# Optimization experiments

Hardware: AMD Instinct MI355X
Metric: run time of the kernel (lower is better)

Reference implementation:

```python
import jax, jax.numpy as jnp
import numpy as np

B, T, C, H = 2, 2048, 1024, 16
HD = C // H  # head dim = 64


def setup_inputs() -> dict:
    key = jax.random.key(0)
    k0, k1, k2 = jax.random.split(key, 3)
    x = jax.random.normal(k0, (B, T, C), jnp.float32)
    W_attn = jax.random.normal(k1, (C, 3 * C), jnp.float32) * 0.02
    b_attn = jnp.zeros((3 * C,), jnp.float32)
    W_proj = jax.random.normal(k2, (C, C), jnp.float32) * 0.02
    b_proj = jnp.zeros((C,), jnp.float32)
    # causal mask, broadcast over (B, H) like torch masked_fill(~mask)
    attn_mask = jnp.tril(jnp.ones((T, T), dtype=bool))[None, None]
    return {"x": x, "W_attn": W_attn, "b_attn": b_attn,
            "W_proj": W_proj, "b_proj": b_proj, "attn_mask": attn_mask}


def _rotate_half(x):
    # interleaved rotate_half as in rotary-embedding-torch: (x1,x2)->(-x2,x1)
    x1 = x[..., 0::2]
    x2 = x[..., 1::2]
    return jnp.stack((-x2, x1), axis=-1).reshape(x.shape)


def _apply_rope(x):
    # x: [B, H, T, HD]
    hd = x.shape[-1]
    t = x.shape[-2]
    inv_freq = 1.0 / (10000.0 ** (jnp.arange(0, hd, 2, dtype=jnp.float32) / hd))
    freqs = jnp.arange(t, dtype=jnp.float32)[:, None] * inv_freq[None, :]  # [T, HD/2]
    freqs = jnp.repeat(freqs, 2, axis=-1)  # [T, HD], interleaved
    return x * jnp.cos(freqs) + _rotate_half(x) * jnp.sin(freqs)


def reference(x, W_attn, b_attn, W_proj, b_proj, attn_mask):
    Bb, Tt, Cc = x.shape
    qkv = x @ W_attn + b_attn                     # [B, T, 3C]
    q, k, v = jnp.split(qkv, 3, axis=-1)

    def to_heads(z):
        return z.reshape(Bb, Tt, H, HD).transpose(0, 2, 1, 3)  # [B, H, T, HD]

    q, k, v = to_heads(q), to_heads(k), to_heads(v)
    q = _apply_rope(q)
    k = _apply_rope(k)

    scale = 1.0 / jnp.sqrt(jnp.float32(HD))
    att = jnp.einsum('bhqd,bhkd->bhqk', q, k) * scale  # [B, H, T, T]
    att = jnp.where(attn_mask, att, jnp.float32(-10000.0))
    att = jax.nn.softmax(att, axis=-1)
    # dropout = 0.0 (eval): identity
    y = jnp.einsum('bhqk,bhkd->bhqd', att, v)           # [B, H, T, HD]
    y = y.transpose(0, 2, 1, 3).reshape(Bb, Tt, Cc)
    return y @ W_proj + b_proj
```

## Files before the change

kernel.cpp:

```cpp
#include <hip/hip_runtime.h>

#define B_ 2
#define T_ 2048
#define C_ 1024
#define H_ 16
#define HD_ 64

typedef unsigned short u16;
typedef unsigned int u32;
typedef __attribute__((ext_vector_type(8))) short short8;
typedef __attribute__((ext_vector_type(4))) float f32x4;
typedef __attribute__((ext_vector_type(2))) u32 uint2v;
typedef __attribute__((ext_vector_type(4))) u32 uint4v;

typedef __attribute__((address_space(1))) const void* as1cv;
typedef __attribute__((address_space(3))) void* as3v;

__device__ __forceinline__ u16 f2bf(float x){
  union { float f; u32 u; } v; v.f = x;
  u32 r = v.u + 0x7fffu + ((v.u >> 16) & 1u);
  return (u16)(r >> 16);
}
__device__ __forceinline__ float bf2f(u16 h){
  union { u32 u; float f; } v; v.u = ((u32)h) << 16;
  return v.f;
}
__device__ __forceinline__ u32 cvt_pk_bf16(float lo, float hi){
  u32 r;
  asm("v_cvt_pk_bf16_f32 %0, %1, %2" : "=v"(r) : "v"(lo), "v"(hi));
  return r;
}
__device__ __forceinline__ void gl_lds16(const u16* src, u16* dst){
  __builtin_amdgcn_global_load_lds((as1cv)src, (as3v)dst, 16, 0, 0);
}

__global__ void k_conv(const float* __restrict__ in, u16* __restrict__ out){
  int i = blockIdx.x * 256 + threadIdx.x;
  f32x4 v = ((const f32x4*)in)[i];
  uint2v o;
  o.x = (u32)f2bf(v.x) | ((u32)f2bf(v.y) << 16);
  o.y = (u32)f2bf(v.z) | ((u32)f2bf(v.w) << 16);
  ((uint2v*)out)[i] = o;
}

__global__ void k_transpose(const float* __restrict__ in, u16* __restrict__ out,
                            int R, int Cc){
  __shared__ float tile[32][33];
  int c0 = blockIdx.x * 32, r0 = blockIdx.y * 32;
  int tx = threadIdx.x, ty = threadIdx.y;
#pragma unroll
  for (int ii = 0; ii < 4; ++ii)
    tile[ty + ii*8][tx] = in[(size_t)(r0 + ty + ii*8) * Cc + c0 + tx];
  __syncthreads();
#pragma unroll
  for (int ii = 0; ii < 4; ++ii)
    out[(size_t)(c0 + ty + ii*8) * R + r0 + tx] = f2bf(tile[tx][ty + ii*8]);
}

__global__ __launch_bounds__(256, 2)
void k_gemm0(const u16* __restrict__ A, const u16* __restrict__ Bt,
             const float* __restrict__ bias, u16* __restrict__ Qh,
             u16* __restrict__ Kh, u16* __restrict__ vt,
             int M, int N, int K)
{
  __shared__ u16 As[128*64];
  __shared__ u16 Bs[128*64];
  int nwg = gridDim.x;
  int cpx = nwg >> 3;
  int bid = blockIdx.x;
  int wg = (bid & 7) * cpx + (bid >> 3);
  int ntn = N >> 7;
  int m0 = (wg / ntn) << 7, n0 = (wg % ntn) << 7;
  int tid = threadIdx.x;
  int lane = tid & 63, w = tid >> 6;
  int c = lane & 15, g = lane >> 4;
  int wr = w >> 1, wc = w & 1;

  f32x4 z4 = {0.f,0.f,0.f,0.f};
  f32x4 acc[4][4];
#pragma unroll
  for (int i=0;i<4;++i)
#pragma unroll
    for (int j=0;j<4;++j) acc[i][j] = z4;

  u16* dstA = As + ((tid & 0xC0) << 3);
  u16* dstB = Bs + ((tid & 0xC0) << 3);

  for (int k0 = 0; k0 < K; k0 += 64){
#pragma unroll
    for (int it = 0; it < 4; ++it){
      int ch = it*256 + tid;
      int row = ch >> 3, slot = ch & 7;
      gl_lds16(A + (size_t)(m0+row)*K + k0 + slot*8, dstA + it*2048);
    }
#pragma unroll
    for (int it = 0; it < 4; ++it){
      int ch = it*256 + tid;
      int row = ch >> 3, slot = ch & 7;
      gl_lds16(Bt + (size_t)(n0+row)*K + k0 + slot*8, dstB + it*2048);
    }
    __syncthreads();
#pragma unroll
    for (int ks = 0; ks < 2; ++ks){
      short8 af[4], bf[4];
#pragma unroll
      for (int i=0;i<4;++i)
        af[i] = *(const short8*)(As + (wr*64 + i*16 + c)*64 + ks*32 + g*8);
#pragma unroll
      for (int j=0;j<4;++j)
        bf[j] = *(const short8*)(Bs + (wc*64 + j*16 + c)*64 + ks*32 + g*8);
#pragma unroll
      for (int i=0;i<4;++i)
#pragma unroll
        for (int j=0;j<4;++j)
          acc[i][j] = __builtin_amdgcn_mfma_f32_16x16x32_bf16(af[i], bf[j], acc[i][j], 0, 0, 0);
    }
    __syncthreads();
  }

  if (n0 >= 2048){
#pragma unroll
    for (int i=0;i<4;++i){
      int rowb = m0 + wr*64 + i*16 + g*4;
      int bb = rowb >> 11, t0 = rowb & 2047;
#pragma unroll
      for (int j=0;j<4;++j){
        int col = n0 + wc*64 + j*16 + c;
        float bv = bias[col];
        int vc = col - 2048;
        int hh = vc >> 6, d = vc & 63;
        uint2v o;
        o.x = (u32)f2bf(acc[i][j].x + bv) | ((u32)f2bf(acc[i][j].y + bv) << 16);
        o.y = (u32)f2bf(acc[i][j].z + bv) | ((u32)f2bf(acc[i][j].w + bv) << 16);
        *(uint2v*)(vt + ((size_t)((bb*16 + hh)*64 + d))*2048 + t0) = o;
      }
    }
  } else {
    bool isQ = (n0 < 1024);
    u16* dsth = isQ ? Qh : Kh;
    int colb = isQ ? n0 : (n0 - 1024);
    float qsc = isQ ? 0.180336880f : 1.0f;
    float sgn = (c & 1) ? 1.f : -1.f;
#pragma unroll
    for (int nf=0; nf<4; ++nf){
      int scol = colb + wc*64 + nf*16 + c;
      int hh = scol >> 6, d = scol & 63;
      int ip = (d >> 1);
      float invr = exp2f((float)(-ip) * 0.4152410118609203f) * 0.15915494309f;
      float bv = bias[n0 + wc*64 + nf*16 + c];
      u16* base = dsth + (size_t)hh*2048*64 + d;
#pragma unroll
      for (int mf=0; mf<4; ++mf){
#pragma unroll
        for (int r=0; r<4; ++r){
          int row = m0 + wr*64 + mf*16 + g*4 + r;
          int t = row & 2047, b = row >> 11;
          float v = acc[mf][nf][r] + bv;
          float p = __shfl_xor(v, 1);
          float th = (float)t * invr;
          float fr = th - floorf(th);
          float sn = __builtin_amdgcn_sinf(fr);
          float cs = __builtin_amdgcn_cosf(fr);
          float y = (v*cs + p*sn*sgn) * qsc;
          base[((size_t)b*16*2048 + t)*64] = f2bf(y);
        }
      }
    }
  }
}

__global__ __launch_bounds__(256, 2)
void k_gemmp(const u16* __restrict__ A, const u16* __restrict__ Bt,
             const float* __restrict__ bias, float* __restrict__ outf)
{
  __shared__ u16 As[128*64];
  __shared__ u16 Bs[64*64];
  const int K = 1024, N = 1024;
  int nwg = gridDim.x;
  int cpx = nwg >> 3;
  int bid = blockIdx.x;
  int wg = (bid & 7) * cpx + (bid >> 3);
  int m0 = (wg >> 4) << 7, n0 = (wg & 15) << 6;
  int tid = threadIdx.x;
  int lane = tid & 63, w = tid >> 6;
  int c = lane & 15, g = lane >> 4;
  int wr = w >> 1, wc = w & 1;

  f32x4 z4 = {0.f,0.f,0.f,0.f};
  f32x4 acc[4][2];
#pragma unroll
  for (int i=0;i<4;++i)
#pragma unroll
    for (int j=0;j<2;++j) acc[i][j] = z4;

  u16* dstA = As + ((tid & 0xC0) << 3);
  u16* dstB = Bs + ((tid & 0xC0) << 3);

  for (int k0 = 0; k0 < K; k0 += 64){
#pragma unroll
    for (int it = 0; it < 4; ++it){
      int ch = it*256 + tid;
      int row = ch >> 3, slot = ch & 7;
      gl_lds16(A + (size_t)(m0+row)*K + k0 + slot*8, dstA + it*2048);
    }
#pragma unroll
    for (int it = 0; it < 2; ++it){
      int ch = it*256 + tid;
      int row = ch >> 3, slot = ch & 7;
      gl_lds16(Bt + (size_t)(n0+row)*K + k0 + slot*8, dstB + it*2048);
    }
    __syncthreads();
#pragma unroll
    for (int ks = 0; ks < 2; ++ks){
      short8 af[4], bf[2];
#pragma unroll
      for (int i=0;i<4;++i)
        af[i] = *(const short8*)(As + (wr*64 + i*16 + c)*64 + ks*32 + g*8);
#pragma unroll
      for (int j=0;j<2;++j)
        bf[j] = *(const short8*)(Bs + (wc*32 + j*16 + c)*64 + ks*32 + g*8);
#pragma unroll
      for (int i=0;i<4;++i)
#pragma unroll
        for (int j=0;j<2;++j)
          acc[i][j] = __builtin_amdgcn_mfma_f32_16x16x32_bf16(af[i], bf[j], acc[i][j], 0, 0, 0);
    }
    __syncthreads();
  }

#pragma unroll
  for (int i=0;i<4;++i){
#pragma unroll
    for (int j=0;j<2;++j){
      int col = n0 + wc*32 + j*16 + c;
      float bv = bias[col];
#pragma unroll
      for (int r=0;r<4;++r){
        int row = m0 + wr*64 + i*16 + g*4 + r;
        outf[(size_t)row*N + col] = acc[i][j][r] + bv;
      }
    }
  }
}

__global__ __launch_bounds__(256, 3)
void k_attn(const u16* __restrict__ Qh, const u16* __restrict__ Kh,
            const u16* __restrict__ Vt, u16* __restrict__ Pb,
            float* __restrict__ lp)
{
  __shared__ u16 KV[4*4096];
  __shared__ u16 Ps[4*32*64];

  int bid = blockIdx.x;
  int qt = 15 - (bid >> 7);
  int r7 = bid & 127;
  int ck = r7 >> 5, bh = r7 & 31;
  int q0 = qt << 7;
  int tid = threadIdx.x, lane = tid & 63, w = tid >> 6;
  int c = lane & 15, g = lane >> 4;
  int q0w = q0 + w*32;
  int nt = (qt + 1) << 1;
  int t0 = (nt * ck) >> 2;
  int t1 = (nt * (ck + 1)) >> 2;

  const u16* Kbase = Kh + (size_t)bh * T_ * 64;
  const u16* Vbase = Vt + (size_t)bh * 64 * T_;
  const u16* Qbase = Qh + (size_t)bh * T_ * 64;

  short8 qf[2][2];
#pragma unroll
  for (int qs=0;qs<2;++qs)
#pragma unroll
    for (int ks=0;ks<2;++ks)
      qf[qs][ks] = *(const short8*)(Qbase + (size_t)(q0w + qs*16 + c)*64 + ks*32 + g*8);

  f32x4 z4 = {0.f,0.f,0.f,0.f};
  f32x4 acc[2][4];
#pragma unroll
  for (int qs=0;qs<2;++qs)
#pragma unroll
    for (int ds=0;ds<4;++ds) acc[qs][ds] = z4;
  float psum[2] = {0.f, 0.f};

  char* PsB = (char*)Ps + w*4096;

  int row2[2], soff2[2];
  u16* dst0[2];
#pragma unroll
  for (int it=0; it<2; ++it){
    int ch = it*256 + tid;
    row2[it] = ch >> 3;
    int slot = ch & 7;
    soff2[it] = (slot ^ (row2[it] & 7)) << 3;
    dst0[it] = KV + ((it*256 + (tid & 0xC0)) << 3);
  }

  if (t0 < t1){
    int kv0 = t0 << 6;
#pragma unroll
    for (int it=0; it<2; ++it){
      gl_lds16(Kbase + (size_t)(kv0 + row2[it])*64 + soff2[it], dst0[it]);
      gl_lds16(Vbase + (size_t)row2[it]*T_ + kv0 + soff2[it], dst0[it] + 2*4096);
    }
  }
  __syncthreads();

  for (int t = t0; t < t1; ++t){
    int cur = (t - t0) & 1;
    int kv0 = t << 6;
    if (t + 1 < t1){
      int kvn = kv0 + 64;
      int nxt = cur ^ 1;
#pragma unroll
      for (int it=0; it<2; ++it){
        gl_lds16(Kbase + (size_t)(kvn + row2[it])*64 + soff2[it], dst0[it] + nxt*4096);
        gl_lds16(Vbase + (size_t)row2[it]*T_ + kvn + soff2[it], dst0[it] + (2+nxt)*4096);
      }
    }

    if (kv0 <= q0w + 31){
      const char* KsC = (const char*)(KV + cur*4096);
      const char* VsC = (const char*)(KV + (2+cur)*4096);

      f32x4 st[4][2];
#pragma unroll
      for (int kv=0;kv<4;++kv)
#pragma unroll
        for (int qs=0;qs<2;++qs) st[kv][qs] = z4;

#pragma unroll
      for (int ks=0;ks<2;++ks){
        short8 kf[4];
#pragma unroll
        for (int kv=0;kv<4;++kv){
          int row = kv*16 + c;
          kf[kv] = *(const short8*)(KsC + row*128 + (((ks*4+g) ^ (row&7)) << 4));
        }
#pragma unroll
        for (int kv=0;kv<4;++kv)
#pragma unroll
          for (int qs=0;qs<2;++qs)
            st[kv][qs] = __builtin_amdgcn_mfma_f32_16x16x32_bf16(kf[kv], qf[qs][ks], st[kv][qs], 0, 0, 0);
      }

      if (kv0 + 63 > q0w){
#pragma unroll
        for (int kv=0;kv<4;++kv)
#pragma unroll
          for (int qs=0;qs<2;++qs)
#pragma unroll
            for (int r=0;r<4;++r){
              int kvi = kv0 + kv*16 + g*4 + r;
              int qi = q0w + qs*16 + c;
              if (kvi > qi) st[kv][qs][r] = -INFINITY;
            }
      }

#pragma unroll
      for (int qs=0;qs<2;++qs){
        float s01 = 0.f, s23 = 0.f;
#pragma unroll
        for (int kv=0;kv<4;++kv){
          float e0 = __builtin_amdgcn_exp2f(st[kv][qs][0]);
          float e1 = __builtin_amdgcn_exp2f(st[kv][qs][1]);
          float e2 = __builtin_amdgcn_exp2f(st[kv][qs][2]);
          float e3 = __builtin_amdgcn_exp2f(st[kv][qs][3]);
          st[kv][qs][0] = e0; st[kv][qs][1] = e1;
          st[kv][qs][2] = e2; st[kv][qs][3] = e3;
          s01 += e0 + e1; s23 += e2 + e3;
        }
        psum[qs] += s01 + s23;
        int q = qs*16 + c;
#pragma unroll
        for (int kv=0;kv<4;++kv){
          uint2v o;
          o.x = cvt_pk_bf16(st[kv][qs][0], st[kv][qs][1]);
          o.y = cvt_pk_bf16(st[kv][qs][2], st[kv][qs][3]);
          *(uint2v*)(PsB + q*128 + ((kv*32 + g*8) ^ ((q&7) << 4))) = o;
        }
      }

#pragma unroll
      for (int ks=0;ks<2;++ks){
        short8 vb[4];
#pragma unroll
        for (int ds=0;ds<4;++ds){
          int row = ds*16 + c;
          vb[ds] = *(const short8*)(VsC + row*128 + (((ks*4+g) ^ (row&7)) << 4));
        }
#pragma unroll
        for (int qs=0;qs<2;++qs){
          int q = qs*16 + c;
          short8 pa = *(const short8*)(PsB + q*128 + (((ks*4+g) << 4) ^ ((q&7) << 4)));
#pragma unroll
          for (int ds=0;ds<4;++ds)
            acc[qs][ds] = __builtin_amdgcn_mfma_f32_16x16x32_bf16(pa, vb[ds], acc[qs][ds], 0, 0, 0);
        }
      }
    }

    __syncthreads();
  }

#pragma unroll
  for (int qs=0;qs<2;++qs){
    psum[qs] += __shfl_xor(psum[qs], 16);
    psum[qs] += __shfl_xor(psum[qs], 32);
  }
  if (g == 0){
    lp[ck*65536 + bh*2048 + q0w + c]      = psum[0];
    lp[ck*65536 + bh*2048 + q0w + 16 + c] = psum[1];
  }
#pragma unroll
  for (int qs=0;qs<2;++qs){
#pragma unroll
    for (int r=0;r<4;++r){
      int trow = q0w + qs*16 + g*4 + r;
      size_t off = (((size_t)(ck*32 + bh)*2048) + trow)*64;
#pragma unroll
      for (int ds=0;ds<4;++ds)
        Pb[off + ds*16 + c] = f2bf(acc[qs][ds][r]);
    }
  }
}

__global__ void k_merge(const u16* __restrict__ Pb, const float* __restrict__ lp,
                        u16* __restrict__ Y)
{
  int idx = blockIdx.x * 256 + threadIdx.x;
  int d8 = idx & 7;
  int t  = (idx >> 3) & 2047;
  int bh = idx >> 14;
  int lt = bh*2048 + t;
  float l = lp[lt] + lp[lt + 65536] + lp[lt + 131072] + lp[lt + 196608];
  float inv = 1.0f / l;
  float s[8] = {0.f,0.f,0.f,0.f,0.f,0.f,0.f,0.f};
#pragma unroll
  for (int ck=0; ck<4; ++ck){
    short8 p = *(const short8*)(Pb + (((size_t)(ck*32 + bh)*2048 + t) << 6) + d8*8);
#pragma unroll
    for (int j=0;j<8;++j) s[j] += bf2f((u16)p[j]);
  }
  uint4v o;
  o.x = cvt_pk_bf16(s[0]*inv, s[1]*inv);
  o.y = cvt_pk_bf16(s[2]*inv, s[3]*inv);
  o.z = cvt_pk_bf16(s[4]*inv, s[5]*inv);
  o.w = cvt_pk_bf16(s[6]*inv, s[7]*inv);
  int bb = bh >> 4, hh = bh & 15;
  *(uint4v*)(Y + ((size_t)(bb*2048 + t))*1024 + hh*64 + d8*8) = o;
}

extern "C" void kernel_launch(void* const* d_in, const int* in_sizes, int n_in,
                              void* d_out, int out_size, void* d_ws, size_t ws_size,
                              hipStream_t stream)
{
  const float* x  = (const float*)d_in[0];
  const float* Wa = (const float*)d_in[1];
  const float* ba = (const float*)d_in[2];
  const float* Wp = (const float*)d_in[3];
  const float* bp = (const float*)d_in[4];
  float* out = (float*)d_out;
  char* ws = (char*)d_ws;

  u16* xb  = (u16*)(ws);
  u16* WaT = (u16*)(ws + (8u  << 20));
  u16* Pb  = (u16*)(ws);
  u16* Qh  = (u16*)(ws + (32u << 20));
  u16* Y   = Qh;
  u16* Kh  = (u16*)(ws + (40u << 20));
  u16* Vt  = (u16*)(ws + (48u << 20));
  u16* WpT = (u16*)(ws + (56u << 20));
  float* lp = (float*)(ws + (58u << 20));

  k_conv<<<4096, 256, 0, stream>>>(x, xb);
  k_transpose<<<dim3(96,32), dim3(32,8), 0, stream>>>(Wa, WaT, 1024, 3072);
  k_transpose<<<dim3(32,32), dim3(32,8), 0, stream>>>(Wp, WpT, 1024, 1024);
  k_gemm0<<<768, 256, 0, stream>>>(xb, WaT, ba, Qh, Kh, Vt, 4096, 3072, 1024);
  k_attn<<<2048, 256, 0, stream>>>(Qh, Kh, Vt, Pb, lp);
  k_merge<<<2048, 256, 0, stream>>>(Pb, lp, Y);
  k_gemmp<<<512, 256, 0, stream>>>(Y, WpT, bp, out);
}
```

Baseline: 111.3 us.

## Double-buffer LDS in both GEMMs and widen projection GEMM tile to 128x128

Both the QKV GEMM and the output-projection GEMM now use two LDS buffers. The next K-slice is loaded from global memory into one buffer while MFMAs consume the other, which removes one barrier per iteration and hides load latency. The projection GEMM also moves from 128x64 to 128x128 tiles with half as many workgroups, which raises operand reuse. In exchange, LDS use doubles to 64KB per block, which may lower occupancy, and the projection launch has only 256 workgroups to spread across the CUs.

```diff
diff --git a/kernel.cpp b/kernel.cpp
--- a/kernel.cpp
+++ b/kernel.cpp
@@ -63,8 +63,7 @@
              u16* __restrict__ Kh, u16* __restrict__ vt,
              int M, int N, int K)
 {
-  __shared__ u16 As[128*64];
-  __shared__ u16 Bs[128*64];
+  __shared__ u16 LDSG[32768];
   int nwg = gridDim.x;
   int cpx = nwg >> 3;
   int bid = blockIdx.x;
@@ -83,23 +82,38 @@
 #pragma unroll
     for (int j=0;j<4;++j) acc[i][j] = z4;
 
-  u16* dstA = As + ((tid & 0xC0) << 3);
-  u16* dstB = Bs + ((tid & 0xC0) << 3);
-
-  for (int k0 = 0; k0 < K; k0 += 64){
-#pragma unroll
-    for (int it = 0; it < 4; ++it){
-      int ch = it*256 + tid;
-      int row = ch >> 3, slot = ch & 7;
-      gl_lds16(A + (size_t)(m0+row)*K + k0 + slot*8, dstA + it*2048);
-    }
-#pragma unroll
-    for (int it = 0; it < 4; ++it){
-      int ch = it*256 + tid;
-      int row = ch >> 3, slot = ch & 7;
-      gl_lds16(Bt + (size_t)(n0+row)*K + k0 + slot*8, dstB + it*2048);
-    }
-    __syncthreads();
+  int rowS[4], slotS[4], dstS[4];
+#pragma unroll
+  for (int it=0; it<4; ++it){
+    int ch = it*256 + tid;
+    rowS[it] = ch >> 3;
+    slotS[it] = (ch & 7) * 8;
+    dstS[it] = it*2048 + ((tid & 0xC0) << 3);
+  }
+  const u16* Abase = A + (size_t)m0*K;
+  const u16* Bbase = Bt + (size_t)n0*K;
+
+#pragma unroll
+  for (int it=0; it<4; ++it){
+    gl_lds16(Abase + (size_t)rowS[it]*K + slotS[it], LDSG + dstS[it]);
+    gl_lds16(Bbase + (size_t)rowS[it]*K + slotS[it], LDSG + 16384 + dstS[it]);
+  }
+  __syncthreads();
+
+  int nk = K >> 6;
+  for (int kt = 0; kt < nk; ++kt){
+    int cur = kt & 1;
+    if (kt + 1 < nk){
+      int k1 = (kt + 1) << 6;
+      int nb = cur ^ 1;
+#pragma unroll
+      for (int it=0; it<4; ++it){
+        gl_lds16(Abase + (size_t)rowS[it]*K + k1 + slotS[it], LDSG + nb*8192 + dstS[it]);
+        gl_lds16(Bbase + (size_t)rowS[it]*K + k1 + slotS[it], LDSG + 16384 + nb*8192 + dstS[it]);
+      }
+    }
+    const u16* As = LDSG + cur*8192;
+    const u16* Bs = LDSG + 16384 + cur*8192;
 #pragma unroll
     for (int ks = 0; ks < 2; ++ks){
       short8 af[4], bf[4];
@@ -173,56 +187,70 @@
 void k_gemmp(const u16* __restrict__ A, const u16* __restrict__ Bt,
              const float* __restrict__ bias, float* __restrict__ outf)
 {
-  __shared__ u16 As[128*64];
-  __shared__ u16 Bs[64*64];
+  __shared__ u16 LDSG[32768];
   const int K = 1024, N = 1024;
   int nwg = gridDim.x;
   int cpx = nwg >> 3;
   int bid = blockIdx.x;
   int wg = (bid & 7) * cpx + (bid >> 3);
-  int m0 = (wg >> 4) << 7, n0 = (wg & 15) << 6;
+  int m0 = (wg >> 3) << 7, n0 = (wg & 7) << 7;
   int tid = threadIdx.x;
   int lane = tid & 63, w = tid >> 6;
   int c = lane & 15, g = lane >> 4;
   int wr = w >> 1, wc = w & 1;
 
   f32x4 z4 = {0.f,0.f,0.f,0.f};
-  f32x4 acc[4][2];
+  f32x4 acc[4][4];
 #pragma unroll
   for (int i=0;i<4;++i)
 #pragma unroll
-    for (int j=0;j<2;++j) acc[i][j] = z4;
-
-  u16* dstA = As + ((tid & 0xC0) << 3);
-  u16* dstB = Bs + ((tid & 0xC0) << 3);
-
-  for (int k0 = 0; k0 < K; k0 += 64){
-#pragma unroll
-    for (int it = 0; it < 4; ++it){
-      int ch = it*256 + tid;
-      int row = ch >> 3, slot = ch & 7;
-      gl_lds16(A + (size_t)(m0+row)*K + k0 + slot*8, dstA + it*2048);
-    }
-#pragma unroll
-    for (int it = 0; it < 2; ++it){
-      int ch = it*256 + tid;
-      int row = ch >> 3, slot = ch & 7;
-      gl_lds16(Bt + (size_t)(n0+row)*K + k0 + slot*8, dstB + it*2048);
-    }
-    __syncthreads();
+    for (int j=0;j<4;++j) acc[i][j] = z4;
+
+  int rowS[4], slotS[4], dstS[4];
+#pragma unroll
+  for (int it=0; it<4; ++it){
+    int ch = it*256 + tid;
+    rowS[it] = ch >> 3;
+    slotS[it] = (ch & 7) * 8;
+    dstS[it] = it*2048 + ((tid & 0xC0) << 3);
+  }
+  const u16* Abase = A + (size_t)m0*K;
+  const u16* Bbase = Bt + (size_t)n0*K;
+
+#pragma unroll
+  for (int it=0; it<4; ++it){
+    gl_lds16(Abase + (size_t)rowS[it]*K + slotS[it], LDSG + dstS[it]);
+    gl_lds16(Bbase + (size_t)rowS[it]*K + slotS[it], LDSG + 16384 + dstS[it]);
+  }
+  __syncthreads();
+
+  const int nk = K >> 6;
+  for (int kt = 0; kt < nk; ++kt){
+    int cur = kt & 1;
+    if (kt + 1 < nk){
+      int k1 = (kt + 1) << 6;
+      int nb = cur ^ 1;
+#pragma unroll
+      for (int it=0; it<4; ++it){
+        gl_lds16(Abase + (size_t)rowS[it]*K + k1 + slotS[it], LDSG + nb*8192 + dstS[it]);
+        gl_lds16(Bbase + (size_t)rowS[it]*K + k1 + slotS[it], LDSG + 16384 + nb*8192 + dstS[it]);
+      }
+    }
+    const u16* As = LDSG + cur*8192;
+    const u16* Bs = LDSG + 16384 + cur*8192;
 #pragma unroll
     for (int ks = 0; ks < 2; ++ks){
-      short8 af[4], bf[2];
+      short8 af[4], bf[4];
 #pragma unroll
       for (int i=0;i<4;++i)
         af[i] = *(const short8*)(As + (wr*64 + i*16 + c)*64 + ks*32 + g*8);
 #pragma unroll
-      for (int j=0;j<2;++j)
-        bf[j] = *(const short8*)(Bs + (wc*32 + j*16 + c)*64 + ks*32 + g*8);
+      for (int j=0;j<4;++j)
+        bf[j] = *(const short8*)(Bs + (wc*64 + j*16 + c)*64 + ks*32 + g*8);
 #pragma unroll
       for (int i=0;i<4;++i)
 #pragma unroll
-        for (int j=0;j<2;++j)
+        for (int j=0;j<4;++j)
           acc[i][j] = __builtin_amdgcn_mfma_f32_16x16x32_bf16(af[i], bf[j], acc[i][j], 0, 0, 0);
     }
     __syncthreads();
@@ -231,8 +259,8 @@
 #pragma unroll
   for (int i=0;i<4;++i){
 #pragma unroll
-    for (int j=0;j<2;++j){
-      int col = n0 + wc*32 + j*16 + c;
+    for (int j=0;j<4;++j){
+      int col = n0 + wc*64 + j*16 + c;
       float bv = bias[col];
 #pragma unroll
       for (int r=0;r<4;++r){
@@ -478,5 +506,5 @@
   k_gemm0<<<768, 256, 0, stream>>>(xb, WaT, ba, Qh, Kh, Vt, 4096, 3072, 1024);
   k_attn<<<2048, 256, 0, stream>>>(Qh, Kh, Vt, Pb, lp);
   k_merge<<<2048, 256, 0, stream>>>(Pb, lp, Y);
-  k_gemmp<<<512, 256, 0, stream>>>(Y, WpT, bp, out);
-}
+  k_gemmp<<<256, 256, 0, stream>>>(Y, WpT, bp, out);
+}
```

After: 117.1 us. 1.05x slower.
